# Optimization experiments

Hardware: AMD Instinct MI355X
Metric: run time of the kernel (lower is better)

## Reference

```python
import jax, jax.numpy as jnp
import numpy as np

B, T = 128, 51            # batch, token sequence length (cond token prepended -> T+1=52)
C, H = 1024, 16           # embed_dim, n_head
L = 8                     # total Blocks: 4 in trans_base + 4 in trans_head
F = 4 * C                 # fc_rate * embed_dim
V = 1024                  # num_vq
CLIP = 512
EPS = 1e-5


def sincos_pe(seq_len, dim):
    # faithful to pos_encoding.PE1d_sincos
    pos = np.arange(seq_len, dtype=np.float32)[:, None]
    div = np.exp(np.arange(0, dim, 2, dtype=np.float32) * (-np.log(10000.0) / dim))
    pe = np.zeros((seq_len, dim), np.float32)
    pe[:, 0::2] = np.sin(pos * div)
    pe[:, 1::2] = np.cos(pos * div)
    return jnp.asarray(pe)


def setup_inputs() -> dict:
    key = jax.random.key(0)
    ks = jax.random.split(key, 12)
    s = 0.02  # init std per _init_weights
    nrm = lambda k, shape: jax.random.normal(k, shape, jnp.float32) * s
    return dict(
        idx=jax.random.randint(ks[0], (B, T), 0, V + 2),
        clip_feature=jax.random.normal(ks[1], (B, CLIP), jnp.float32),
        tok_emb=nrm(ks[2], (V + 2, C)),
        cond_w=nrm(ks[3], (CLIP, C)), cond_b=jnp.zeros((C,), jnp.float32),
        ln1_w=jnp.ones((L, C), jnp.float32), ln1_b=jnp.zeros((L, C), jnp.float32),
        wq=nrm(ks[4], (L, C, C)), bq=jnp.zeros((L, C), jnp.float32),
        wk=nrm(ks[5], (L, C, C)), bk=jnp.zeros((L, C), jnp.float32),
        wv=nrm(ks[6], (L, C, C)), bv=jnp.zeros((L, C), jnp.float32),
        wp=nrm(ks[7], (L, C, C)), bp=jnp.zeros((L, C), jnp.float32),
        ln2_w=jnp.ones((L, C), jnp.float32), ln2_b=jnp.zeros((L, C), jnp.float32),
        w1=nrm(ks[8], (L, C, F)), b1=jnp.zeros((L, F), jnp.float32),
        w2=nrm(ks[9], (L, F, C)), b2=jnp.zeros((L, C), jnp.float32),
        lnf_w=jnp.ones((C,), jnp.float32), lnf_b=jnp.zeros((C,), jnp.float32),
        head_w=nrm(ks[10], (C, V + 1)),
    )


def _ln(x, w, b):
    m = jnp.mean(x, axis=-1, keepdims=True)
    v = jnp.var(x, axis=-1, keepdims=True)
    return (x - m) * jax.lax.rsqrt(v + EPS) * w + b


def _block(x, ln1w, ln1b, wq, bq, wk, bk, wv, bv, wp, bp, ln2w, ln2b, w1, b1, w2, b2):
    b_, t_, c_ = x.shape
    d = c_ // H
    h = _ln(x, ln1w, ln1b)
    q = (h @ wq + bq).reshape(b_, t_, H, d).transpose(0, 2, 1, 3)  # [B,H,T,d]
    k = (h @ wk + bk).reshape(b_, t_, H, d).transpose(0, 2, 1, 3)
    v = (h @ wv + bv).reshape(b_, t_, H, d).transpose(0, 2, 1, 3)
    att = jnp.einsum('bhqd,bhkd->bhqk', q, k) * (1.0 / np.sqrt(d))
    causal = jnp.tril(jnp.ones((t_, t_), bool))
    att = jnp.where(causal, att, -jnp.inf)
    att = jax.nn.softmax(att, axis=-1)
    y = jnp.einsum('bhqk,bhkd->bhqd', att, v).transpose(0, 2, 1, 3).reshape(b_, t_, c_)
    x = x + y @ wp + bp
    h2 = _ln(x, ln2w, ln2b)
    x = x + jax.nn.gelu(h2 @ w1 + b1, approximate=False) @ w2 + b2
    return x


def reference(idx, clip_feature, tok_emb, cond_w, cond_b,
              ln1_w, ln1_b, wq, bq, wk, bk, wv, bv, wp, bp,
              ln2_w, ln2_b, w1, b1, w2, b2, lnf_w, lnf_b, head_w):
    # CrossCondTransBase: cond token + token embeddings + sinusoidal pos embed
    cond = (clip_feature @ cond_w + cond_b)[:, None, :]           # [B,1,C]
    tok = tok_emb[idx]                                            # [B,T,C]
    x = jnp.concatenate([cond, tok], axis=1)                      # [B,T+1,C]
    x = x + sincos_pe(x.shape[1], C)[None, :, :]
    # 4 base blocks + 4 head blocks (identical structure, stacked params)
    for i in range(L):
        x = _block(x, ln1_w[i], ln1_b[i], wq[i], bq[i], wk[i], bk[i],
                   wv[i], bv[i], wp[i], bp[i], ln2_w[i], ln2_b[i],
                   w1[i], b1[i], w2[i], b2[i])
    x = _ln(x, lnf_w, lnf_b)
    logits = x @ head_w                                           # [B,T+1,num_vq+1]
    return logits
```

## Files before the change

kernel.cpp:

```cpp
#include <hip/hip_runtime.h>

using bf16x8 = __attribute__((ext_vector_type(8))) __bf16;
using short8 = __attribute__((ext_vector_type(8))) short;
using u16x8  = __attribute__((ext_vector_type(8))) unsigned short;
using u16x4  = __attribute__((ext_vector_type(4))) unsigned short;
using f32x4  = __attribute__((ext_vector_type(4))) float;

#define DEVI __device__ __forceinline__

DEVI unsigned short f2bf(float f) {
  union { float f; unsigned u; } un; un.f = f;
  unsigned r = un.u + 0x7fffu + ((un.u >> 16) & 1u);
  return (unsigned short)(r >> 16);
}

typedef const __attribute__((address_space(1))) void* gas1_t;
typedef __attribute__((address_space(3))) void* las3_t;

DEVI void gload16(const void* g, void* lds) {
  __builtin_amdgcn_global_load_lds(
      reinterpret_cast<gas1_t>(reinterpret_cast<unsigned long long>(g)),
      reinterpret_cast<las3_t>(static_cast<unsigned>(reinterpret_cast<unsigned long long>(lds))),
      16, 0, 0);
}

__global__ void __launch_bounds__(256)
transpose_cvt(const float* __restrict__ src, unsigned short* __restrict__ dst,
              int K, int N, int Nrows, long srcStride, long dstStride) {
  src += (size_t)blockIdx.z * srcStride;
  dst += (size_t)blockIdx.z * dstStride;
  __shared__ float tile[32][33];
  const int n0 = blockIdx.x * 32, k0 = blockIdx.y * 32;
  const int tx = threadIdx.x & 31, ty = threadIdx.x >> 5;
#pragma unroll
  for (int i = 0; i < 4; ++i) {
    const int kk = ty + i * 8;
    const int n = n0 + tx;
    tile[kk][tx] = (n < N) ? src[(size_t)(k0 + kk) * N + n] : 0.f;
  }
  __syncthreads();
#pragma unroll
  for (int i = 0; i < 4; ++i) {
    const int nn = ty + i * 8;
    const int n = n0 + nn;
    if (n < Nrows) dst[(size_t)n * K + k0 + tx] = f2bf(tile[tx][nn]);
  }
}

__global__ void __launch_bounds__(256)
concat_bias(const float* __restrict__ bq, const float* __restrict__ bk,
            const float* __restrict__ bv, float* __restrict__ ob) {
  const int i = blockIdx.x * 256 + threadIdx.x;
  if (i >= 8 * 3072) return;
  const int l = i / 3072, c = i - l * 3072;
  float v;
  if (c < 1024)      v = bq[l * 1024 + c];
  else if (c < 2048) v = bk[l * 1024 + c - 1024];
  else               v = bv[l * 1024 + c - 2048];
  ob[i] = v;
}

__global__ void __launch_bounds__(256)
embed_kernel(const int* __restrict__ idx, const float* __restrict__ clip,
             const float* __restrict__ tok_emb, const float* __restrict__ cond_w,
             const float* __restrict__ cond_b, float* __restrict__ x) {
  const int row = blockIdx.x;
  const int b = row / 52, t = row - b * 52;
  const int c0 = threadIdx.x * 4;
  float e[4];
  if (t == 0) {
    e[0] = cond_b[c0]; e[1] = cond_b[c0 + 1]; e[2] = cond_b[c0 + 2]; e[3] = cond_b[c0 + 3];
    for (int k = 0; k < 512; ++k) {
      const float cf = clip[b * 512 + k];
      const float4 wv = *(const float4*)&cond_w[k * 1024 + c0];
      e[0] += cf * wv.x; e[1] += cf * wv.y; e[2] += cf * wv.z; e[3] += cf * wv.w;
    }
  } else {
    const int tok = idx[b * 51 + t - 1];
    const float4 tv = *(const float4*)&tok_emb[(size_t)tok * 1024 + c0];
    e[0] = tv.x; e[1] = tv.y; e[2] = tv.z; e[3] = tv.w;
  }
  const float nl = -9.2103403719761836f / 1024.0f;
#pragma unroll
  for (int j = 0; j < 4; ++j) {
    const int c = c0 + j;
    const float dv = expf((float)(c & ~1) * nl);
    const float ang = (float)t * dv;
    e[j] += (c & 1) ? cosf(ang) : sinf(ang);
  }
  float4 o; o.x = e[0]; o.y = e[1]; o.z = e[2]; o.w = e[3];
  *(float4*)&x[(size_t)row * 1024 + c0] = o;
}

__global__ void __launch_bounds__(256)
ln_kernel(const float* __restrict__ x, const float* __restrict__ w,
          const float* __restrict__ bsh, unsigned short* __restrict__ out) {
  const size_t row = blockIdx.x;
  const int tid = threadIdx.x;
  const float4 v = *(const float4*)&x[row * 1024 + tid * 4];
  float s1 = v.x + v.y + v.z + v.w;
  float s2 = v.x * v.x + v.y * v.y + v.z * v.z + v.w * v.w;
#pragma unroll
  for (int m = 1; m < 64; m <<= 1) { s1 += __shfl_xor(s1, m); s2 += __shfl_xor(s2, m); }
  __shared__ float red[8];
  const int wid = tid >> 6;
  if ((tid & 63) == 0) { red[wid] = s1; red[4 + wid] = s2; }
  __syncthreads();
  s1 = red[0] + red[1] + red[2] + red[3];
  s2 = red[4] + red[5] + red[6] + red[7];
  const float mean = s1 * (1.0f / 1024.0f);
  const float var  = s2 * (1.0f / 1024.0f) - mean * mean;
  const float rstd = rsqrtf(var + 1e-5f);
  const float4 wv = *(const float4*)&w[tid * 4];
  const float4 bv = *(const float4*)&bsh[tid * 4];
  ushort4 o;
  o.x = f2bf((v.x - mean) * rstd * wv.x + bv.x);
  o.y = f2bf((v.y - mean) * rstd * wv.y + bv.y);
  o.z = f2bf((v.z - mean) * rstd * wv.z + bv.z);
  o.w = f2bf((v.w - mean) * rstd * wv.w + bv.w);
  *(ushort4*)&out[row * 1024 + tid * 4] = o;
}

__global__ void __launch_bounds__(256)
ln_sum_kernel(const float* __restrict__ xold, const float* __restrict__ part,
              long pstride, int S, const float* __restrict__ fcb,
              const float* __restrict__ w, const float* __restrict__ bsh,
              float* __restrict__ xnew, unsigned short* __restrict__ hout) {
  const size_t row = blockIdx.x;
  const int tid = threadIdx.x;
  const float4 xv = *(const float4*)&xold[row * 1024 + tid * 4];
  const float4 bb = *(const float4*)&fcb[tid * 4];
  float e0 = xv.x + bb.x, e1 = xv.y + bb.y, e2 = xv.z + bb.z, e3 = xv.w + bb.w;
  for (int s = 0; s < S; ++s) {
    const float4 p = *(const float4*)&part[(size_t)s * pstride + row * 1024 + tid * 4];
    e0 += p.x; e1 += p.y; e2 += p.z; e3 += p.w;
  }
  float s1 = e0 + e1 + e2 + e3;
  float s2 = e0 * e0 + e1 * e1 + e2 * e2 + e3 * e3;
#pragma unroll
  for (int m = 1; m < 64; m <<= 1) { s1 += __shfl_xor(s1, m); s2 += __shfl_xor(s2, m); }
  __shared__ float red[8];
  const int wid = tid >> 6;
  if ((tid & 63) == 0) { red[wid] = s1; red[4 + wid] = s2; }
  __syncthreads();
  s1 = red[0] + red[1] + red[2] + red[3];
  s2 = red[4] + red[5] + red[6] + red[7];
  const float mean = s1 * (1.0f / 1024.0f);
  const float var  = s2 * (1.0f / 1024.0f) - mean * mean;
  const float rstd = rsqrtf(var + 1e-5f);
  float4 xo; xo.x = e0; xo.y = e1; xo.z = e2; xo.w = e3;
  *(float4*)&xnew[row * 1024 + tid * 4] = xo;
  const float4 wv = *(const float4*)&w[tid * 4];
  const float4 bv = *(const float4*)&bsh[tid * 4];
  ushort4 o;
  o.x = f2bf((e0 - mean) * rstd * wv.x + bv.x);
  o.y = f2bf((e1 - mean) * rstd * wv.y + bv.y);
  o.z = f2bf((e2 - mean) * rstd * wv.z + bv.z);
  o.w = f2bf((e3 - mean) * rstd * wv.w + bv.w);
  *(ushort4*)&hout[row * 1024 + tid * 4] = o;
}

template <int EPI>
__global__ void __launch_bounds__(512, 2)
gemm256(const unsigned short* __restrict__ A, const unsigned short* __restrict__ WT,
        const float* __restrict__ bias, void* outp,
        int Kfull, int N, int k_len, int ny, int nz) {
  constexpr bool SWAP = (EPI == 0 || EPI == 1);
  __shared__ unsigned short smem[65536];
  const int tid = threadIdx.x;
  const int lane = tid & 63;
  const int wid = tid >> 6;
  const int lrow = lane & 15, lkg = lane >> 4;
  const int wm = wid >> 2, wn = wid & 3;

  const int nwg = gridDim.x;
  int bid = blockIdx.x;
  {
    const int q = nwg >> 3, r = nwg & 7;
    const int xcd = bid & 7, i = bid >> 3;
    bid = ((xcd < r) ? xcd * (q + 1) : r * (q + 1) + (xcd - r) * q) + i;
  }
  const int nxy = nwg / nz;
  const int z = bid / nxy;
  const int rem = bid - z * nxy;
  const int xt = rem / ny;
  const int yt = rem - xt * ny;
  const long m0 = (long)xt * 256;
  const long n0 = (long)yt * 256;
  const int kb = z * k_len;

  const unsigned short* ag[2];
  const unsigned short* bg[2];
#pragma unroll
  for (int j = 0; j < 2; ++j) {
    const int c = tid + j * 512;
    const int f = c >> 6, kg = (c >> 4) & 3, r = c & 15;
    ag[j] = A  + (m0 + f * 16 + r) * (long)Kfull + kb + kg * 8;
    bg[j] = WT + (n0 + f * 16 + r) * (long)Kfull + kb + kg * 8;
  }
  const int lo0 = wid * 512;
  const int lo1 = 4096 + wid * 512;

  f32x4 acc[8][4] = {};
  const int T = k_len >> 5;

  auto STAGE = [&](int t) {
    const int bo = (t & 3) * 16384;
    const int kt = t * 32;
    gload16(ag[0] + kt, smem + bo + lo0);
    gload16(ag[1] + kt, smem + bo + lo1);
    gload16(bg[0] + kt, smem + bo + 8192 + lo0);
    gload16(bg[1] + kt, smem + bo + 8192 + lo1);
  };

  STAGE(0); STAGE(1); STAGE(2);

  for (int t = 0; t < T; ++t) {
    if (t < T - 2)      asm volatile("s_waitcnt vmcnt(8)" ::: "memory");
    else if (t < T - 1) asm volatile("s_waitcnt vmcnt(4)" ::: "memory");
    else                asm volatile("s_waitcnt vmcnt(0)" ::: "memory");
    __builtin_amdgcn_s_barrier();
    __builtin_amdgcn_sched_barrier(0);
    if (t + 3 < T) STAGE(t + 3);
    const int ca = (t & 3) * 16384;
    const int cB = ca + 8192;
    bf16x8 bfr[4], afr[4];
#pragma unroll
    for (int n = 0; n < 4; ++n) bfr[n] = *(const bf16x8*)&smem[cB + (wn * 4 + n) * 512 + lane * 8];
#pragma unroll
    for (int m = 0; m < 4; ++m) afr[m] = *(const bf16x8*)&smem[ca + (wm * 8 + m) * 512 + lane * 8];
    asm volatile("s_waitcnt lgkmcnt(0)" ::: "memory");
    __builtin_amdgcn_sched_barrier(0);
    __builtin_amdgcn_s_setprio(1);
#pragma unroll
    for (int m = 0; m < 4; ++m)
#pragma unroll
      for (int n = 0; n < 4; ++n) {
        if constexpr (SWAP)
          acc[m][n] = __builtin_amdgcn_mfma_f32_16x16x32_bf16(bfr[n], afr[m], acc[m][n], 0, 0, 0);
        else
          acc[m][n] = __builtin_amdgcn_mfma_f32_16x16x32_bf16(afr[m], bfr[n], acc[m][n], 0, 0, 0);
      }
    __builtin_amdgcn_s_setprio(0);
    __builtin_amdgcn_s_barrier();
#pragma unroll
    for (int m = 0; m < 4; ++m) afr[m] = *(const bf16x8*)&smem[ca + (wm * 8 + 4 + m) * 512 + lane * 8];
    asm volatile("s_waitcnt lgkmcnt(0)" ::: "memory");
    __builtin_amdgcn_sched_barrier(0);
    __builtin_amdgcn_s_setprio(1);
#pragma unroll
    for (int m = 0; m < 4; ++m)
#pragma unroll
      for (int n = 0; n < 4; ++n) {
        if constexpr (SWAP)
          acc[4 + m][n] = __builtin_amdgcn_mfma_f32_16x16x32_bf16(bfr[n], afr[m], acc[4 + m][n], 0, 0, 0);
        else
          acc[4 + m][n] = __builtin_amdgcn_mfma_f32_16x16x32_bf16(afr[m], bfr[n], acc[4 + m][n], 0, 0, 0);
      }
    __builtin_amdgcn_s_setprio(0);
  }
  __syncthreads();

  if constexpr (SWAP) {
#pragma unroll
    for (int m = 0; m < 8; ++m) {
      const int row = wm * 128 + m * 16 + lrow;
      const unsigned rb = (unsigned)row * 512;
      const unsigned sw = (unsigned)(row & 7) << 4;
#pragma unroll
      for (int n = 0; n < 4; ++n) {
        const int colb = wn * 64 + n * 16 + lkg * 4;
        const float4 bv = *(const float4*)&bias[n0 + colb];
        float v0 = acc[m][n][0] + bv.x;
        float v1 = acc[m][n][1] + bv.y;
        float v2 = acc[m][n][2] + bv.z;
        float v3 = acc[m][n][3] + bv.w;
        if constexpr (EPI == 1) {
          v0 = 0.5f * v0 * (1.0f + erff(v0 * 0.70710678118654752f));
          v1 = 0.5f * v1 * (1.0f + erff(v1 * 0.70710678118654752f));
          v2 = 0.5f * v2 * (1.0f + erff(v2 * 0.70710678118654752f));
          v3 = 0.5f * v3 * (1.0f + erff(v3 * 0.70710678118654752f));
        }
        u16x4 o = { f2bf(v0), f2bf(v1), f2bf(v2), f2bf(v3) };
        *(u16x4*)((char*)smem + ((rb + colb * 2) ^ sw)) = o;
      }
    }
    __syncthreads();
    unsigned short* out = (unsigned short*)outp;
#pragma unroll
    for (int i = 0; i < 16; ++i) {
      const int idx = tid + i * 512;
      const int row = idx >> 5, c32 = idx & 31;
      const unsigned byteoff = ((unsigned)row * 512 + (unsigned)c32 * 16) ^ ((unsigned)(row & 7) << 4);
      const u16x8 v = *(const u16x8*)((const char*)smem + byteoff);
      *(u16x8*)&out[(m0 + row) * (long)N + n0 + c32 * 8] = v;
    }
  } else {
    float* out = (float*)outp + (size_t)z * ((size_t)(nxy / ny) * 256) * N;
#pragma unroll
    for (int n = 0; n < 4; ++n) {
      const int col = (int)n0 + wn * 64 + n * 16 + lrow;
#pragma unroll
      for (int m = 0; m < 8; ++m) {
        const long rowb = m0 + wm * 128 + m * 16 + lkg * 4;
#pragma unroll
        for (int r = 0; r < 4; ++r)
          out[(rowb + r) * (long)N + col] = acc[m][n][r];
      }
    }
  }
}

template <int EPI>
__global__ void __launch_bounds__(256)
gemm128(const unsigned short* __restrict__ A, const unsigned short* __restrict__ WT,
        const float* __restrict__ bias, const float* res, void* outp,
        int Kfull, int N, int k_len, int ny, int nz) {
  __shared__ unsigned short smem[24576];
  const int tid = threadIdx.x;
  const int lane = tid & 63;
  const int wid = tid >> 6;
  const int lrow = lane & 15, lkg = lane >> 4;
  const int wr = wid >> 1, wc = wid & 1;

  const int nwg = gridDim.x;
  int bid = blockIdx.x;
  {
    const int q = nwg >> 3, r = nwg & 7;
    const int xcd = bid & 7, i = bid >> 3;
    bid = ((xcd < r) ? xcd * (q + 1) : r * (q + 1) + (xcd - r) * q) + i;
  }
  const int nxy = nwg / nz;
  const int z = bid / nxy;
  const int rem = bid - z * nxy;
  const int xt = rem / ny;
  const int yt = rem - xt * ny;
  const long m0 = (long)xt * 128;
  const long n0 = (long)yt * 128;
  const int kb = z * k_len;

  const unsigned short* a0 = A + (m0 + (wid * 2 + 0) * 16 + lrow) * (long)Kfull + kb + lkg * 8;
  const unsigned short* a1 = A + (m0 + (wid * 2 + 1) * 16 + lrow) * (long)Kfull + kb + lkg * 8;
  const unsigned short* b0 = WT + (n0 + (wid * 2 + 0) * 16 + lrow) * (long)Kfull + kb + lkg * 8;
  const unsigned short* b1 = WT + (n0 + (wid * 2 + 1) * 16 + lrow) * (long)Kfull + kb + lkg * 8;
  const int so0 = (wid * 2 + 0) * 512, so1 = (wid * 2 + 1) * 512;

  f32x4 acc[4][4] = {};
  const int T = k_len >> 5;

  auto STAGE = [&](int t) {
    const int boff = (t % 3) * 8192;
    const int kt = t * 32;
    gload16(a0 + kt, smem + boff + so0);
    gload16(a1 + kt, smem + boff + so1);
    gload16(b0 + kt, smem + boff + 4096 + so0);
    gload16(b1 + kt, smem + boff + 4096 + so1);
  };

  STAGE(0);
  STAGE(1);

  for (int t = 0; t < T; ++t) {
    if (t + 1 < T) asm volatile("s_waitcnt vmcnt(4)" ::: "memory");
    else           asm volatile("s_waitcnt vmcnt(0)" ::: "memory");
    __builtin_amdgcn_s_barrier();
    __builtin_amdgcn_sched_barrier(0);
    if (t + 2 < T) STAGE(t + 2);
    const int cb = (t % 3) * 8192;
    bf16x8 af[4], bf8[4];
#pragma unroll
    for (int m = 0; m < 4; ++m) af[m] = *(const bf16x8*)&smem[cb + (wr * 4 + m) * 512 + lane * 8];
#pragma unroll
    for (int n = 0; n < 4; ++n) bf8[n] = *(const bf16x8*)&smem[cb + 4096 + (wc * 4 + n) * 512 + lane * 8];
#pragma unroll
    for (int m = 0; m < 4; ++m)
#pragma unroll
      for (int n = 0; n < 4; ++n)
        acc[m][n] = __builtin_amdgcn_mfma_f32_16x16x32_bf16(af[m], bf8[n], acc[m][n], 0, 0, 0);
  }
  __syncthreads();

#pragma unroll
  for (int n = 0; n < 4; ++n) {
    const int col = (int)n0 + wc * 64 + n * 16 + lrow;
    const bool cv = col < N;
    float bv = 0.f;
    if (EPI == 2) bv = cv ? bias[col] : 0.f;
#pragma unroll
    for (int m = 0; m < 4; ++m) {
      const long rowb = m0 + wr * 64 + m * 16 + lkg * 4;
#pragma unroll
      for (int r = 0; r < 4; ++r) {
        float v = acc[m][n][r] + bv;
        if (cv) {
          if constexpr (EPI == 2)
            ((float*)outp)[(rowb + r) * (long)N + col] = res[(rowb + r) * (long)N + col] + v;
          else
            ((float*)outp)[(rowb + r) * (long)N + col] = v;
        }
      }
    }
  }
}

__global__ void __launch_bounds__(256)
attn_kernel(const unsigned short* __restrict__ qkv,
            unsigned short* __restrict__ attno) {
  __shared__ unsigned short qA[4096];
  __shared__ unsigned short kB[4096];
  __shared__ unsigned short vB[4096];
  __shared__ unsigned short pA[4096];
  const int bh = blockIdx.x;
  const int b = bh >> 4, h = bh & 15;
  const int tid = threadIdx.x;
  const int lane = tid & 63;
  const int wid = tid >> 6;
  const int lrow = lane & 15, lkg = lane >> 4;

  for (int i = tid; i < 512; i += 256) {
    const int row = i >> 3;
    const int dc = i & 7;
    short8 qv = {}, kv = {}, vv = {};
    if (row < 52) {
      const unsigned short* base = qkv + ((size_t)(b * 52 + row)) * 3072 + h * 64 + dc * 8;
      qv = *(const short8*)(base);
      kv = *(const short8*)(base + 1024);
      vv = *(const short8*)(base + 2048);
    }
    *(short8*)&qA[(row >> 4) * 1024 + dc * 128 + (row & 15) * 8] = qv;
    *(short8*)&kB[(row >> 4) * 1024 + dc * 128 + (row & 15) * 8] = kv;
#pragma unroll
    for (int j = 0; j < 8; ++j) {
      const int d = dc * 8 + j;
      vB[(d >> 4) * 1024 + (row >> 3) * 128 + (d & 15) * 8 + (row & 7)] = (unsigned short)vv[j];
    }
  }
  __syncthreads();

  f32x4 sacc[4] = {};
#pragma unroll
  for (int s = 0; s < 2; ++s) {
    const bf16x8 a = *(const bf16x8*)&qA[wid * 1024 + s * 512 + lane * 8];
#pragma unroll
    for (int c = 0; c < 4; ++c) {
      const bf16x8 bb = *(const bf16x8*)&kB[c * 1024 + s * 512 + lane * 8];
      sacc[c] = __builtin_amdgcn_mfma_f32_16x16x32_bf16(a, bb, sacc[c], 0, 0, 0);
    }
  }

#pragma unroll
  for (int r = 0; r < 4; ++r) {
    const int trow = wid * 16 + lkg * 4 + r;
    float sv[4];
#pragma unroll
    for (int c = 0; c < 4; ++c) {
      const int kp = c * 16 + lrow;
      sv[c] = (kp <= trow && kp < 52) ? sacc[c][r] * 0.125f : -3.0e38f;
    }
    float mx = fmaxf(fmaxf(sv[0], sv[1]), fmaxf(sv[2], sv[3]));
#pragma unroll
    for (int m = 1; m < 16; m <<= 1) mx = fmaxf(mx, __shfl_xor(mx, m));
    float p[4], sum = 0.f;
#pragma unroll
    for (int c = 0; c < 4; ++c) { p[c] = __expf(sv[c] - mx); sum += p[c]; }
#pragma unroll
    for (int m = 1; m < 16; m <<= 1) sum += __shfl_xor(sum, m);
    const float inv = 1.0f / sum;
#pragma unroll
    for (int c = 0; c < 4; ++c) {
      const int kp = c * 16 + lrow;
      pA[wid * 1024 + (kp >> 3) * 128 + (lkg * 4 + r) * 8 + (kp & 7)] = f2bf(p[c] * inv);
    }
  }
  __syncthreads();

  f32x4 oacc[4] = {};
#pragma unroll
  for (int s = 0; s < 2; ++s) {
    const bf16x8 a = *(const bf16x8*)&pA[wid * 1024 + s * 512 + lane * 8];
#pragma unroll
    for (int db = 0; db < 4; ++db) {
      const bf16x8 bb = *(const bf16x8*)&vB[db * 1024 + s * 512 + lane * 8];
      oacc[db] = __builtin_amdgcn_mfma_f32_16x16x32_bf16(a, bb, oacc[db], 0, 0, 0);
    }
  }
#pragma unroll
  for (int db = 0; db < 4; ++db)
#pragma unroll
    for (int r = 0; r < 4; ++r) {
      const int trow = wid * 16 + lkg * 4 + r;
      if (trow < 52) {
        const int d = db * 16 + lrow;
        attno[((size_t)(b * 52 + trow)) * 1024 + h * 64 + d] = f2bf(oacc[db][r]);
      }
    }
}

extern "C" void kernel_launch(void* const* d_in, const int* in_sizes, int n_in,
                              void* d_out, int out_size, void* d_ws, size_t ws_size,
                              hipStream_t stream) {
  const int*   idx    = (const int*)d_in[0];
  const float* clip   = (const float*)d_in[1];
  const float* tok    = (const float*)d_in[2];
  const float* cond_w = (const float*)d_in[3];
  const float* cond_b = (const float*)d_in[4];
  const float* ln1w   = (const float*)d_in[5];
  const float* ln1b   = (const float*)d_in[6];
  const float* wq     = (const float*)d_in[7];
  const float* bq     = (const float*)d_in[8];
  const float* wk     = (const float*)d_in[9];
  const float* bk     = (const float*)d_in[10];
  const float* wv     = (const float*)d_in[11];
  const float* bv     = (const float*)d_in[12];
  const float* wp     = (const float*)d_in[13];
  const float* bp     = (const float*)d_in[14];
  const float* ln2w   = (const float*)d_in[15];
  const float* ln2b   = (const float*)d_in[16];
  const float* w1     = (const float*)d_in[17];
  const float* b1     = (const float*)d_in[18];
  const float* w2     = (const float*)d_in[19];
  const float* b2     = (const float*)d_in[20];
  const float* lnfw   = (const float*)d_in[21];
  const float* lnfb   = (const float*)d_in[22];
  const float* headw  = (const float*)d_in[23];

  const int M = 6656;
  char* ws = (char*)d_ws;
  size_t off = 0;
  auto alloc = [&](size_t bytes) -> void* {
    void* p = ws + off;
    off += (bytes + 255) & ~(size_t)255;
    return p;
  };

  unsigned short* qkvT  = (unsigned short*)alloc((size_t)8 * 3072 * 1024 * 2);
  unsigned short* wpT   = (unsigned short*)alloc((size_t)8 * 1024 * 1024 * 2);
  unsigned short* w1T   = (unsigned short*)alloc((size_t)8 * 4096 * 1024 * 2);
  unsigned short* w2T   = (unsigned short*)alloc((size_t)8 * 1024 * 4096 * 2);
  unsigned short* headT = (unsigned short*)alloc((size_t)1152 * 1024 * 2);
  float*          qkvB  = (float*)alloc((size_t)8 * 3072 * 4);
  float*          xbuf  = (float*)alloc((size_t)M * 1024 * 4);
  unsigned short* hbuf  = (unsigned short*)alloc((size_t)M * 1024 * 2);
  unsigned short* big   = (unsigned short*)alloc((size_t)M * 4096 * 2);
  unsigned short* attno = (unsigned short*)alloc((size_t)M * 1024 * 2);
  float*          pbuf  = (float*)alloc((size_t)2 * M * 1024 * 4);
  unsigned short* qkv  = big;
  unsigned short* mlph = big;
  const long ps1024 = (long)M * 1024;

  const dim3 tb(256);
  const dim3 tb512(512);
  transpose_cvt<<<dim3(32, 32, 8), tb, 0, stream>>>(wq, qkvT,                        1024, 1024, 1024, (long)1024 * 1024, (long)3072 * 1024);
  transpose_cvt<<<dim3(32, 32, 8), tb, 0, stream>>>(wk, qkvT + (size_t)1024 * 1024,  1024, 1024, 1024, (long)1024 * 1024, (long)3072 * 1024);
  transpose_cvt<<<dim3(32, 32, 8), tb, 0, stream>>>(wv, qkvT + (size_t)2048 * 1024,  1024, 1024, 1024, (long)1024 * 1024, (long)3072 * 1024);
  transpose_cvt<<<dim3(32, 32, 8), tb, 0, stream>>>(wp, wpT,  1024, 1024, 1024, (long)1024 * 1024, (long)1024 * 1024);
  transpose_cvt<<<dim3(128, 32, 8), tb, 0, stream>>>(w1, w1T, 1024, 4096, 4096, (long)1024 * 4096, (long)4096 * 1024);
  transpose_cvt<<<dim3(32, 128, 8), tb, 0, stream>>>(w2, w2T, 4096, 1024, 1024, (long)4096 * 1024, (long)1024 * 4096);
  transpose_cvt<<<dim3(36, 32, 1), tb, 0, stream>>>(headw, headT, 1024, 1025, 1152, 0, 0);
  concat_bias<<<dim3(96), tb, 0, stream>>>(bq, bk, bv, qkvB);
  embed_kernel<<<dim3(M), tb, 0, stream>>>(idx, clip, tok, cond_w, cond_b, xbuf);
  ln_kernel<<<dim3(M), tb, 0, stream>>>(xbuf, ln1w, ln1b, hbuf);

  for (int l = 0; l < 8; ++l) {
    gemm256<0><<<dim3(312), tb512, 0, stream>>>(hbuf, qkvT + (size_t)l * 3072 * 1024,
                                                qkvB + l * 3072, qkv, 1024, 3072, 1024, 12, 1);
    attn_kernel<<<dim3(2048), tb, 0, stream>>>(qkv, attno);
    gemm128<2><<<dim3(52 * 8), tb, 0, stream>>>(attno, wpT + (size_t)l * 1024 * 1024,
                                                bp + l * 1024, xbuf, xbuf, 1024, 1024, 1024, 8, 1);
    ln_kernel<<<dim3(M), tb, 0, stream>>>(xbuf, ln2w + l * 1024, ln2b + l * 1024, hbuf);
    gemm256<1><<<dim3(416), tb512, 0, stream>>>(hbuf, w1T + (size_t)l * 4096 * 1024,
                                                b1 + l * 4096, mlph, 1024, 4096, 1024, 16, 1);
    gemm256<4><<<dim3(208), tb512, 0, stream>>>(mlph, w2T + (size_t)l * 1024 * 4096,
                                                nullptr, pbuf, 4096, 1024, 2048, 4, 2);
    if (l < 7)
      ln_sum_kernel<<<dim3(M), tb, 0, stream>>>(xbuf, pbuf, ps1024, 2, b2 + l * 1024,
                                                ln1w + (l + 1) * 1024, ln1b + (l + 1) * 1024, xbuf, hbuf);
    else
      ln_sum_kernel<<<dim3(M), tb, 0, stream>>>(xbuf, pbuf, ps1024, 2, b2 + l * 1024,
                                                lnfw, lnfb, xbuf, hbuf);
  }
  gemm128<3><<<dim3(52 * 9), tb, 0, stream>>>(hbuf, headT, nullptr, nullptr, d_out, 1024, 1025, 1024, 9, 1);
}
```

Measured before the change: 3.067 ms.

## Restructure GEMM main loop into 64-wide K steps with double-buffered interleaved loads

Replaces the 4-stage, 32-wide K pipeline with a 2-buffer scheme where each iteration covers 64 K elements split into four 16-MFMA phases. Global-to-LDS loads for later tiles are issued in chunks between phases, with barriers separating LDS reads from compute, in the style of ping-pong scheduling. The aim is to overlap memory traffic with MFMA work more evenly and to halve loop overhead per K. It adds more barriers per iteration and relies on careful vmcnt accounting, so any error in that accounting could introduce races.

```diff
diff --git a/kernel.cpp b/kernel.cpp
--- a/kernel.cpp
+++ b/kernel.cpp
@@ -23,6 +23,10 @@
       reinterpret_cast<las3_t>(static_cast<unsigned>(reinterpret_cast<unsigned long long>(lds))),
       16, 0, 0);
 }
+
+#define VMW(n) asm volatile("s_waitcnt vmcnt(" #n ")" ::: "memory")
+#define LGK0   do { asm volatile("s_waitcnt lgkmcnt(0)" ::: "memory"); __builtin_amdgcn_sched_barrier(0); } while (0)
+#define BARS   do { __builtin_amdgcn_s_barrier(); __builtin_amdgcn_sched_barrier(0); } while (0)
 
 __global__ void __launch_bounds__(256)
 transpose_cvt(const float* __restrict__ src, unsigned short* __restrict__ dst,
@@ -189,76 +193,85 @@
   const long n0 = (long)yt * 256;
   const int kb = z * k_len;
 
-  const unsigned short* ag[2];
-  const unsigned short* bg[2];
-#pragma unroll
-  for (int j = 0; j < 2; ++j) {
-    const int c = tid + j * 512;
-    const int f = c >> 6, kg = (c >> 4) & 3, r = c & 15;
-    ag[j] = A  + (m0 + f * 16 + r) * (long)Kfull + kb + kg * 8;
-    bg[j] = WT + (n0 + f * 16 + r) * (long)Kfull + kb + kg * 8;
-  }
-  const int lo0 = wid * 512;
-  const int lo1 = 4096 + wid * 512;
+  const int cp = tid >> 6, ckg = (tid >> 4) & 3, cr = tid & 15;
+  auto srcA = [&](int pbase) {
+    const int p = pbase + cp;
+    const int ks = p >> 4, mq = (p >> 3) & 1, wh = (p >> 2) & 1, i = p & 3;
+    const int f = wh * 8 + mq * 4 + i;
+    return A + (m0 + f * 16 + cr) * (long)Kfull + kb + ks * 32 + ckg * 8;
+  };
+  auto srcB = [&](int pbase) {
+    const int p = pbase + cp;
+    const int ks = p >> 4, f = p & 15;
+    return WT + (n0 + f * 16 + cr) * (long)Kfull + kb + ks * 32 + ckg * 8;
+  };
+  const unsigned short *sA0 = srcA(0), *sA2 = srcA(8), *sA3 = srcA(16), *sA5 = srcA(24);
+  const unsigned short *sB1a = srcB(0), *sB1b = srcB(8), *sB4a = srcB(16), *sB4b = srcB(24);
+
+  auto ST = [&](const unsigned short* s, int tt, int ldsb) {
+    gload16(s + (long)tt * 64, smem + (tt & 1) * 32768 + ldsb + wid * 512);
+  };
 
   f32x4 acc[8][4] = {};
-  const int T = k_len >> 5;
-
-  auto STAGE = [&](int t) {
-    const int bo = (t & 3) * 16384;
-    const int kt = t * 32;
-    gload16(ag[0] + kt, smem + bo + lo0);
-    gload16(ag[1] + kt, smem + bo + lo1);
-    gload16(bg[0] + kt, smem + bo + 8192 + lo0);
-    gload16(bg[1] + kt, smem + bo + 8192 + lo1);
-  };
-
-  STAGE(0); STAGE(1); STAGE(2);
+  const int T = k_len >> 6;
+
+#define READ_A(KS, MQ) do { _Pragma("unroll") \
+  for (int i = 0; i < 4; ++i) \
+    afr[i] = *(const bf16x8*)&smem[bo + ((KS) * 16 + (MQ) * 8 + wm * 4 + i) * 512 + lane * 8]; \
+  } while (0)
+#define READ_B(KS, DST) do { _Pragma("unroll") \
+  for (int n = 0; n < 4; ++n) \
+    DST[n] = *(const bf16x8*)&smem[bo + 16384 + ((KS) * 16 + wn * 4 + n) * 512 + lane * 8]; \
+  } while (0)
+#define MFMA16(AB, BF) do { \
+  __builtin_amdgcn_s_setprio(1); \
+  _Pragma("unroll") \
+  for (int mm = 0; mm < 4; ++mm) { \
+    _Pragma("unroll") \
+    for (int nn = 0; nn < 4; ++nn) { \
+      if constexpr (SWAP) \
+        acc[(AB) + mm][nn] = __builtin_amdgcn_mfma_f32_16x16x32_bf16(BF[nn], afr[mm], acc[(AB) + mm][nn], 0, 0, 0); \
+      else \
+        acc[(AB) + mm][nn] = __builtin_amdgcn_mfma_f32_16x16x32_bf16(afr[mm], BF[nn], acc[(AB) + mm][nn], 0, 0, 0); \
+    } \
+  } \
+  __builtin_amdgcn_s_setprio(0); \
+} while (0)
+
+  ST(sA0, 0, 0);  ST(sB1a, 0, 16384); ST(sB1b, 0, 20480); ST(sA2, 0, 4096);
+  ST(sA3, 0, 8192); ST(sB4a, 0, 24576); ST(sB4b, 0, 28672); ST(sA5, 0, 12288);
+  ST(sA0, 1, 0);  ST(sB1a, 1, 16384); ST(sB1b, 1, 20480); ST(sA2, 1, 4096);
+  ST(sA3, 1, 8192); ST(sB4a, 1, 24576); ST(sB4b, 1, 28672);
+  VMW(7); BARS;
 
   for (int t = 0; t < T; ++t) {
-    if (t < T - 2)      asm volatile("s_waitcnt vmcnt(8)" ::: "memory");
-    else if (t < T - 1) asm volatile("s_waitcnt vmcnt(4)" ::: "memory");
-    else                asm volatile("s_waitcnt vmcnt(0)" ::: "memory");
-    __builtin_amdgcn_s_barrier();
-    __builtin_amdgcn_sched_barrier(0);
-    if (t + 3 < T) STAGE(t + 3);
-    const int ca = (t & 3) * 16384;
-    const int cB = ca + 8192;
-    bf16x8 bfr[4], afr[4];
-#pragma unroll
-    for (int n = 0; n < 4; ++n) bfr[n] = *(const bf16x8*)&smem[cB + (wn * 4 + n) * 512 + lane * 8];
-#pragma unroll
-    for (int m = 0; m < 4; ++m) afr[m] = *(const bf16x8*)&smem[ca + (wm * 8 + m) * 512 + lane * 8];
-    asm volatile("s_waitcnt lgkmcnt(0)" ::: "memory");
-    __builtin_amdgcn_sched_barrier(0);
-    __builtin_amdgcn_s_setprio(1);
-#pragma unroll
-    for (int m = 0; m < 4; ++m)
-#pragma unroll
-      for (int n = 0; n < 4; ++n) {
-        if constexpr (SWAP)
-          acc[m][n] = __builtin_amdgcn_mfma_f32_16x16x32_bf16(bfr[n], afr[m], acc[m][n], 0, 0, 0);
-        else
-          acc[m][n] = __builtin_amdgcn_mfma_f32_16x16x32_bf16(afr[m], bfr[n], acc[m][n], 0, 0, 0);
-      }
-    __builtin_amdgcn_s_setprio(0);
-    __builtin_amdgcn_s_barrier();
-#pragma unroll
-    for (int m = 0; m < 4; ++m) afr[m] = *(const bf16x8*)&smem[ca + (wm * 8 + 4 + m) * 512 + lane * 8];
-    asm volatile("s_waitcnt lgkmcnt(0)" ::: "memory");
-    __builtin_amdgcn_sched_barrier(0);
-    __builtin_amdgcn_s_setprio(1);
-#pragma unroll
-    for (int m = 0; m < 4; ++m)
-#pragma unroll
-      for (int n = 0; n < 4; ++n) {
-        if constexpr (SWAP)
-          acc[4 + m][n] = __builtin_amdgcn_mfma_f32_16x16x32_bf16(bfr[n], afr[m], acc[4 + m][n], 0, 0, 0);
-        else
-          acc[4 + m][n] = __builtin_amdgcn_mfma_f32_16x16x32_bf16(afr[m], bfr[n], acc[4 + m][n], 0, 0, 0);
-      }
-    __builtin_amdgcn_s_setprio(0);
-  }
+    const int bo = (t & 1) * 32768;
+    bf16x8 afr[4], bfr0[4], bfr1[4];
+    READ_A(0, 0); READ_B(0, bfr0);
+    if (t + 1 < T) ST(sA5, t + 1, 12288);
+    BARS; LGK0;
+    MFMA16(0, bfr0);
+    BARS;
+    READ_A(0, 1);
+    if (t + 2 < T) { ST(sA0, t + 2, 0); ST(sB1a, t + 2, 16384); ST(sB1b, t + 2, 20480); }
+    BARS; LGK0;
+    MFMA16(4, bfr0);
+    BARS;
+    READ_A(1, 0); READ_B(1, bfr1);
+    if (t + 2 < T) ST(sA2, t + 2, 4096);
+    BARS; LGK0;
+    MFMA16(0, bfr1);
+    BARS;
+    READ_A(1, 1);
+    if (t + 2 < T) { ST(sA3, t + 2, 8192); ST(sB4a, t + 2, 24576); ST(sB4b, t + 2, 28672); }
+    BARS; LGK0;
+    MFMA16(4, bfr1);
+    if (t + 1 < T) { if (t + 2 < T) VMW(7); else VMW(0); }
+    BARS;
+  }
+#undef READ_A
+#undef READ_B
+#undef MFMA16
   __syncthreads();
 
   if constexpr (SWAP) {
```

New measurement: 3.097 ms. No clear change (+1.0%).

## Shrink gemm256 M-tile to 128 rows with 3-stage LDS pipeline for higher occupancy

Applied to the files above, without the earlier changes.

The big GEMM kernel now computes a 128x256 output tile per workgroup instead of 256x256. It uses a 3-deep LDS ring (72KB) instead of a 4-deep one (128KB) and allows 4 waves per SIMD instead of 2. Grid sizes double to cover the same matrices, and the epilogues and split-K output offsets are adjusted to match. The aim is more resident workgroups and better CU fill for M=6656. The cost is lower arithmetic intensity per tile, more B-matrix reloads from memory, and a shallower prefetch depth.

```diff
diff --git a/kernel.cpp b/kernel.cpp
--- a/kernel.cpp
+++ b/kernel.cpp
@@ -23,6 +23,10 @@
       reinterpret_cast<las3_t>(static_cast<unsigned>(reinterpret_cast<unsigned long long>(lds))),
       16, 0, 0);
 }
+
+#define VMW(n) asm volatile("s_waitcnt vmcnt(" #n ")" ::: "memory")
+#define LGK0   do { asm volatile("s_waitcnt lgkmcnt(0)" ::: "memory"); __builtin_amdgcn_sched_barrier(0); } while (0)
+#define BARS   do { __builtin_amdgcn_s_barrier(); __builtin_amdgcn_sched_barrier(0); } while (0)
 
 __global__ void __launch_bounds__(256)
 transpose_cvt(const float* __restrict__ src, unsigned short* __restrict__ dst,
@@ -161,12 +165,12 @@
 }
 
 template <int EPI>
-__global__ void __launch_bounds__(512, 2)
+__global__ void __launch_bounds__(512, 4)
 gemm256(const unsigned short* __restrict__ A, const unsigned short* __restrict__ WT,
         const float* __restrict__ bias, void* outp,
         int Kfull, int N, int k_len, int ny, int nz) {
   constexpr bool SWAP = (EPI == 0 || EPI == 1);
-  __shared__ unsigned short smem[65536];
+  __shared__ unsigned short smem[36864];
   const int tid = threadIdx.x;
   const int lane = tid & 63;
   const int wid = tid >> 6;
@@ -185,52 +189,41 @@
   const int rem = bid - z * nxy;
   const int xt = rem / ny;
   const int yt = rem - xt * ny;
-  const long m0 = (long)xt * 256;
+  const long m0 = (long)xt * 128;
   const long n0 = (long)yt * 256;
   const int kb = z * k_len;
 
-  const unsigned short* ag[2];
-  const unsigned short* bg[2];
-#pragma unroll
-  for (int j = 0; j < 2; ++j) {
-    const int c = tid + j * 512;
-    const int f = c >> 6, kg = (c >> 4) & 3, r = c & 15;
-    ag[j] = A  + (m0 + f * 16 + r) * (long)Kfull + kb + kg * 8;
-    bg[j] = WT + (n0 + f * 16 + r) * (long)Kfull + kb + kg * 8;
-  }
-  const int lo0 = wid * 512;
-  const int lo1 = 4096 + wid * 512;
-
-  f32x4 acc[8][4] = {};
+  const int cr = tid & 15, ckg = (tid >> 4) & 3;
+  const unsigned short* pA  = A  + (m0 + wid * 16 + cr) * (long)Kfull + kb + ckg * 8;
+  const unsigned short* pB0 = WT + (n0 + wid * 16 + cr) * (long)Kfull + kb + ckg * 8;
+  const unsigned short* pB1 = WT + (n0 + 128 + wid * 16 + cr) * (long)Kfull + kb + ckg * 8;
+  const int lo = wid * 512;
+
+  f32x4 acc[4][4] = {};
   const int T = k_len >> 5;
 
   auto STAGE = [&](int t) {
-    const int bo = (t & 3) * 16384;
-    const int kt = t * 32;
-    gload16(ag[0] + kt, smem + bo + lo0);
-    gload16(ag[1] + kt, smem + bo + lo1);
-    gload16(bg[0] + kt, smem + bo + 8192 + lo0);
-    gload16(bg[1] + kt, smem + bo + 8192 + lo1);
+    const int bo = (t % 3) * 12288;
+    const long kt = (long)t * 32;
+    gload16(pA + kt, smem + bo + lo);
+    gload16(pB0 + kt, smem + bo + 4096 + lo);
+    gload16(pB1 + kt, smem + bo + 8192 + lo);
   };
 
-  STAGE(0); STAGE(1); STAGE(2);
+  STAGE(0); STAGE(1);
 
   for (int t = 0; t < T; ++t) {
-    if (t < T - 2)      asm volatile("s_waitcnt vmcnt(8)" ::: "memory");
-    else if (t < T - 1) asm volatile("s_waitcnt vmcnt(4)" ::: "memory");
-    else                asm volatile("s_waitcnt vmcnt(0)" ::: "memory");
-    __builtin_amdgcn_s_barrier();
-    __builtin_amdgcn_sched_barrier(0);
-    if (t + 3 < T) STAGE(t + 3);
-    const int ca = (t & 3) * 16384;
-    const int cB = ca + 8192;
-    bf16x8 bfr[4], afr[4];
-#pragma unroll
-    for (int n = 0; n < 4; ++n) bfr[n] = *(const bf16x8*)&smem[cB + (wn * 4 + n) * 512 + lane * 8];
-#pragma unroll
-    for (int m = 0; m < 4; ++m) afr[m] = *(const bf16x8*)&smem[ca + (wm * 8 + m) * 512 + lane * 8];
-    asm volatile("s_waitcnt lgkmcnt(0)" ::: "memory");
-    __builtin_amdgcn_sched_barrier(0);
+    if (t + 1 < T) VMW(3);
+    else           VMW(0);
+    BARS;
+    if (t + 2 < T) STAGE(t + 2);
+    const int bo = (t % 3) * 12288;
+    bf16x8 afr[4], bfr[4];
+#pragma unroll
+    for (int m = 0; m < 4; ++m) afr[m] = *(const bf16x8*)&smem[bo + (wm * 4 + m) * 512 + lane * 8];
+#pragma unroll
+    for (int n = 0; n < 4; ++n) bfr[n] = *(const bf16x8*)&smem[bo + 4096 + (wn * 4 + n) * 512 + lane * 8];
+    LGK0;
     __builtin_amdgcn_s_setprio(1);
 #pragma unroll
     for (int m = 0; m < 4; ++m)
@@ -242,29 +235,13 @@
           acc[m][n] = __builtin_amdgcn_mfma_f32_16x16x32_bf16(afr[m], bfr[n], acc[m][n], 0, 0, 0);
       }
     __builtin_amdgcn_s_setprio(0);
-    __builtin_amdgcn_s_barrier();
-#pragma unroll
-    for (int m = 0; m < 4; ++m) afr[m] = *(const bf16x8*)&smem[ca + (wm * 8 + 4 + m) * 512 + lane * 8];
-    asm volatile("s_waitcnt lgkmcnt(0)" ::: "memory");
-    __builtin_amdgcn_sched_barrier(0);
-    __builtin_amdgcn_s_setprio(1);
-#pragma unroll
-    for (int m = 0; m < 4; ++m)
-#pragma unroll
-      for (int n = 0; n < 4; ++n) {
-        if constexpr (SWAP)
-          acc[4 + m][n] = __builtin_amdgcn_mfma_f32_16x16x32_bf16(bfr[n], afr[m], acc[4 + m][n], 0, 0, 0);
-        else
-          acc[4 + m][n] = __builtin_amdgcn_mfma_f32_16x16x32_bf16(afr[m], bfr[n], acc[4 + m][n], 0, 0, 0);
-      }
-    __builtin_amdgcn_s_setprio(0);
   }
   __syncthreads();
 
   if constexpr (SWAP) {
 #pragma unroll
-    for (int m = 0; m < 8; ++m) {
-      const int row = wm * 128 + m * 16 + lrow;
+    for (int m = 0; m < 4; ++m) {
+      const int row = wm * 64 + m * 16 + lrow;
       const unsigned rb = (unsigned)row * 512;
       const unsigned sw = (unsigned)(row & 7) << 4;
 #pragma unroll
@@ -288,7 +265,7 @@
     __syncthreads();
     unsigned short* out = (unsigned short*)outp;
 #pragma unroll
-    for (int i = 0; i < 16; ++i) {
+    for (int i = 0; i < 8; ++i) {
       const int idx = tid + i * 512;
       const int row = idx >> 5, c32 = idx & 31;
       const unsigned byteoff = ((unsigned)row * 512 + (unsigned)c32 * 16) ^ ((unsigned)(row & 7) << 4);
@@ -296,13 +273,13 @@
       *(u16x8*)&out[(m0 + row) * (long)N + n0 + c32 * 8] = v;
     }
   } else {
-    float* out = (float*)outp + (size_t)z * ((size_t)(nxy / ny) * 256) * N;
+    float* out = (float*)outp + (size_t)z * ((size_t)(nxy / ny) * 128) * N;
 #pragma unroll
     for (int n = 0; n < 4; ++n) {
       const int col = (int)n0 + wn * 64 + n * 16 + lrow;
 #pragma unroll
-      for (int m = 0; m < 8; ++m) {
-        const long rowb = m0 + wm * 128 + m * 16 + lkg * 4;
+      for (int m = 0; m < 4; ++m) {
+        const long rowb = m0 + wm * 64 + m * 16 + lkg * 4;
 #pragma unroll
         for (int r = 0; r < 4; ++r)
           out[(rowb + r) * (long)N + col] = acc[m][n][r];
@@ -562,15 +539,15 @@
   ln_kernel<<<dim3(M), tb, 0, stream>>>(xbuf, ln1w, ln1b, hbuf);
 
   for (int l = 0; l < 8; ++l) {
-    gemm256<0><<<dim3(312), tb512, 0, stream>>>(hbuf, qkvT + (size_t)l * 3072 * 1024,
+    gemm256<0><<<dim3(624), tb512, 0, stream>>>(hbuf, qkvT + (size_t)l * 3072 * 1024,
                                                 qkvB + l * 3072, qkv, 1024, 3072, 1024, 12, 1);
     attn_kernel<<<dim3(2048), tb, 0, stream>>>(qkv, attno);
     gemm128<2><<<dim3(52 * 8), tb, 0, stream>>>(attno, wpT + (size_t)l * 1024 * 1024,
                                                 bp + l * 1024, xbuf, xbuf, 1024, 1024, 1024, 8, 1);
     ln_kernel<<<dim3(M), tb, 0, stream>>>(xbuf, ln2w + l * 1024, ln2b + l * 1024, hbuf);
-    gemm256<1><<<dim3(416), tb512, 0, stream>>>(hbuf, w1T + (size_t)l * 4096 * 1024,
+    gemm256<1><<<dim3(832), tb512, 0, stream>>>(hbuf, w1T + (size_t)l * 4096 * 1024,
                                                 b1 + l * 4096, mlph, 1024, 4096, 1024, 16, 1);
-    gemm256<4><<<dim3(208), tb512, 0, stream>>>(mlph, w2T + (size_t)l * 1024 * 4096,
+    gemm256<4><<<dim3(416), tb512, 0, stream>>>(mlph, w2T + (size_t)l * 1024 * 4096,
                                                 nullptr, pbuf, 4096, 1024, 2048, 4, 2);
     if (l < 7)
       ln_sum_kernel<<<dim3(M), tb, 0, stream>>>(xbuf, pbuf, ps1024, 2, b2 + l * 1024,
```

Result: slower. 3.174 ms (+3.5%).

## Use 3-stage LDS pipeline, single MFMA phase per k-step, and N-major tile order

Applied to the files above, without the earlier changes.

Shrinks the 256x256 GEMM LDS ring from 4 to 3 stages (96KB instead of 128KB) and prefetches two tiles ahead instead of three. It loads all 8 A fragments at once and drops the mid-iteration barrier, so each k-step runs as one 32-MFMA phase. The epilogue now stages the output through the smaller LDS in two halves. Both GEMM kernels also map block IDs so that consecutive blocks walk M first within a fixed N tile, which should improve weight-tile reuse in cache. The goal is fewer barriers, lower LDS use and better L2 locality, at the cost of a shallower prefetch and more VGPRs held for A fragments.

```diff
diff --git a/kernel.cpp b/kernel.cpp
--- a/kernel.cpp
+++ b/kernel.cpp
@@ -23,6 +23,10 @@
       reinterpret_cast<las3_t>(static_cast<unsigned>(reinterpret_cast<unsigned long long>(lds))),
       16, 0, 0);
 }
+
+#define VMW(n) asm volatile("s_waitcnt vmcnt(" #n ")" ::: "memory")
+#define LGK0   do { asm volatile("s_waitcnt lgkmcnt(0)" ::: "memory"); __builtin_amdgcn_sched_barrier(0); } while (0)
+#define BARS   do { __builtin_amdgcn_s_barrier(); __builtin_amdgcn_sched_barrier(0); } while (0)
 
 __global__ void __launch_bounds__(256)
 transpose_cvt(const float* __restrict__ src, unsigned short* __restrict__ dst,
@@ -166,7 +170,7 @@
         const float* __restrict__ bias, void* outp,
         int Kfull, int N, int k_len, int ny, int nz) {
   constexpr bool SWAP = (EPI == 0 || EPI == 1);
-  __shared__ unsigned short smem[65536];
+  __shared__ unsigned short smem[49152];
   const int tid = threadIdx.x;
   const int lane = tid & 63;
   const int wid = tid >> 6;
@@ -183,8 +187,9 @@
   const int nxy = nwg / nz;
   const int z = bid / nxy;
   const int rem = bid - z * nxy;
-  const int xt = rem / ny;
-  const int yt = rem - xt * ny;
+  const int nx = nxy / ny;
+  const int yt = rem / nx;
+  const int xt = rem - yt * nx;
   const long m0 = (long)xt * 256;
   const long n0 = (long)yt * 256;
   const int kb = z * k_len;
@@ -205,35 +210,31 @@
   const int T = k_len >> 5;
 
   auto STAGE = [&](int t) {
-    const int bo = (t & 3) * 16384;
-    const int kt = t * 32;
+    const int bo = (t % 3) * 16384;
+    const long kt = (long)t * 32;
     gload16(ag[0] + kt, smem + bo + lo0);
     gload16(ag[1] + kt, smem + bo + lo1);
     gload16(bg[0] + kt, smem + bo + 8192 + lo0);
     gload16(bg[1] + kt, smem + bo + 8192 + lo1);
   };
 
-  STAGE(0); STAGE(1); STAGE(2);
+  STAGE(0); STAGE(1);
 
   for (int t = 0; t < T; ++t) {
-    if (t < T - 2)      asm volatile("s_waitcnt vmcnt(8)" ::: "memory");
-    else if (t < T - 1) asm volatile("s_waitcnt vmcnt(4)" ::: "memory");
-    else                asm volatile("s_waitcnt vmcnt(0)" ::: "memory");
-    __builtin_amdgcn_s_barrier();
-    __builtin_amdgcn_sched_barrier(0);
-    if (t + 3 < T) STAGE(t + 3);
-    const int ca = (t & 3) * 16384;
-    const int cB = ca + 8192;
-    bf16x8 bfr[4], afr[4];
-#pragma unroll
-    for (int n = 0; n < 4; ++n) bfr[n] = *(const bf16x8*)&smem[cB + (wn * 4 + n) * 512 + lane * 8];
-#pragma unroll
-    for (int m = 0; m < 4; ++m) afr[m] = *(const bf16x8*)&smem[ca + (wm * 8 + m) * 512 + lane * 8];
-    asm volatile("s_waitcnt lgkmcnt(0)" ::: "memory");
-    __builtin_amdgcn_sched_barrier(0);
+    if (t + 1 < T) VMW(4);
+    else           VMW(0);
+    BARS;
+    if (t + 2 < T) STAGE(t + 2);
+    const int bo = (t % 3) * 16384;
+    bf16x8 afr[8], bfr[4];
+#pragma unroll
+    for (int m = 0; m < 8; ++m) afr[m] = *(const bf16x8*)&smem[bo + (wm * 8 + m) * 512 + lane * 8];
+#pragma unroll
+    for (int n = 0; n < 4; ++n) bfr[n] = *(const bf16x8*)&smem[bo + 8192 + (wn * 4 + n) * 512 + lane * 8];
+    LGK0;
     __builtin_amdgcn_s_setprio(1);
 #pragma unroll
-    for (int m = 0; m < 4; ++m)
+    for (int m = 0; m < 8; ++m)
 #pragma unroll
       for (int n = 0; n < 4; ++n) {
         if constexpr (SWAP)
@@ -242,58 +243,47 @@
           acc[m][n] = __builtin_amdgcn_mfma_f32_16x16x32_bf16(afr[m], bfr[n], acc[m][n], 0, 0, 0);
       }
     __builtin_amdgcn_s_setprio(0);
-    __builtin_amdgcn_s_barrier();
-#pragma unroll
-    for (int m = 0; m < 4; ++m) afr[m] = *(const bf16x8*)&smem[ca + (wm * 8 + 4 + m) * 512 + lane * 8];
-    asm volatile("s_waitcnt lgkmcnt(0)" ::: "memory");
-    __builtin_amdgcn_sched_barrier(0);
-    __builtin_amdgcn_s_setprio(1);
-#pragma unroll
-    for (int m = 0; m < 4; ++m)
-#pragma unroll
-      for (int n = 0; n < 4; ++n) {
-        if constexpr (SWAP)
-          acc[4 + m][n] = __builtin_amdgcn_mfma_f32_16x16x32_bf16(bfr[n], afr[m], acc[4 + m][n], 0, 0, 0);
-        else
-          acc[4 + m][n] = __builtin_amdgcn_mfma_f32_16x16x32_bf16(afr[m], bfr[n], acc[4 + m][n], 0, 0, 0);
+  }
+
+  if constexpr (SWAP) {
+#pragma unroll
+    for (int p = 0; p < 2; ++p) {
+      __syncthreads();
+      if (wm == p) {
+#pragma unroll
+        for (int m = 0; m < 8; ++m) {
+          const int rowl = m * 16 + lrow;
+          const unsigned rb = (unsigned)rowl * 512;
+          const unsigned sw = (unsigned)(rowl & 7) << 4;
+#pragma unroll
+          for (int n = 0; n < 4; ++n) {
+            const int colb = wn * 64 + n * 16 + lkg * 4;
+            const float4 bv = *(const float4*)&bias[n0 + colb];
+            float v0 = acc[m][n][0] + bv.x;
+            float v1 = acc[m][n][1] + bv.y;
+            float v2 = acc[m][n][2] + bv.z;
+            float v3 = acc[m][n][3] + bv.w;
+            if constexpr (EPI == 1) {
+              v0 = 0.5f * v0 * (1.0f + erff(v0 * 0.70710678118654752f));
+              v1 = 0.5f * v1 * (1.0f + erff(v1 * 0.70710678118654752f));
+              v2 = 0.5f * v2 * (1.0f + erff(v2 * 0.70710678118654752f));
+              v3 = 0.5f * v3 * (1.0f + erff(v3 * 0.70710678118654752f));
+            }
+            u16x4 o = { f2bf(v0), f2bf(v1), f2bf(v2), f2bf(v3) };
+            *(u16x4*)((char*)smem + ((rb + colb * 2) ^ sw)) = o;
+          }
+        }
       }
-    __builtin_amdgcn_s_setprio(0);
-  }
-  __syncthreads();
-
-  if constexpr (SWAP) {
-#pragma unroll
-    for (int m = 0; m < 8; ++m) {
-      const int row = wm * 128 + m * 16 + lrow;
-      const unsigned rb = (unsigned)row * 512;
-      const unsigned sw = (unsigned)(row & 7) << 4;
-#pragma unroll
-      for (int n = 0; n < 4; ++n) {
-        const int colb = wn * 64 + n * 16 + lkg * 4;
-        const float4 bv = *(const float4*)&bias[n0 + colb];
-        float v0 = acc[m][n][0] + bv.x;
-        float v1 = acc[m][n][1] + bv.y;
-        float v2 = acc[m][n][2] + bv.z;
-        float v3 = acc[m][n][3] + bv.w;
-        if constexpr (EPI == 1) {
-          v0 = 0.5f * v0 * (1.0f + erff(v0 * 0.70710678118654752f));
-          v1 = 0.5f * v1 * (1.0f + erff(v1 * 0.70710678118654752f));
-          v2 = 0.5f * v2 * (1.0f + erff(v2 * 0.70710678118654752f));
-          v3 = 0.5f * v3 * (1.0f + erff(v3 * 0.70710678118654752f));
-        }
-        u16x4 o = { f2bf(v0), f2bf(v1), f2bf(v2), f2bf(v3) };
-        *(u16x4*)((char*)smem + ((rb + colb * 2) ^ sw)) = o;
+      __syncthreads();
+      unsigned short* out = (unsigned short*)outp;
+#pragma unroll
+      for (int i = 0; i < 8; ++i) {
+        const int idx = tid + i * 512;
+        const int rowl = idx >> 5, c32 = idx & 31;
+        const unsigned byteoff = ((unsigned)rowl * 512 + (unsigned)c32 * 16) ^ ((unsigned)(rowl & 7) << 4);
+        const u16x8 v = *(const u16x8*)((const char*)smem + byteoff);
+        *(u16x8*)&out[(m0 + p * 128 + rowl) * (long)N + n0 + c32 * 8] = v;
       }
-    }
-    __syncthreads();
-    unsigned short* out = (unsigned short*)outp;
-#pragma unroll
-    for (int i = 0; i < 16; ++i) {
-      const int idx = tid + i * 512;
-      const int row = idx >> 5, c32 = idx & 31;
-      const unsigned byteoff = ((unsigned)row * 512 + (unsigned)c32 * 16) ^ ((unsigned)(row & 7) << 4);
-      const u16x8 v = *(const u16x8*)((const char*)smem + byteoff);
-      *(u16x8*)&out[(m0 + row) * (long)N + n0 + c32 * 8] = v;
     }
   } else {
     float* out = (float*)outp + (size_t)z * ((size_t)(nxy / ny) * 256) * N;
@@ -333,8 +323,9 @@
   const int nxy = nwg / nz;
   const int z = bid / nxy;
   const int rem = bid - z * nxy;
-  const int xt = rem / ny;
-  const int yt = rem - xt * ny;
+  const int nx = nxy / ny;
+  const int yt = rem / nx;
+  const int xt = rem - yt * nx;
   const long m0 = (long)xt * 128;
   const long n0 = (long)yt * 128;
   const int kb = z * k_len;
```

After: 3.305 ms. 7.8% more time.
